# Kernel optimization log

Hardware: AMD Instinct MI355X
Metric: run time of the kernel (lower is better)

## Reference

```python
import jax, jax.numpy as jnp
import numpy as np

D_MODEL = 1024
NUM_HEADS = 16
D_K = D_MODEL // NUM_HEADS
SCALE = float(np.sqrt(D_K))


def setup_inputs() -> dict:
    key = jax.random.key(0)
    ks = jax.random.split(key, 11)
    B, S, D = 4, 2048, D_MODEL
    w_std = 1.0 / np.sqrt(D)
    inp = {
        "query": jax.random.normal(ks[0], (B, S, D), jnp.float32),
        "key": jax.random.normal(ks[1], (B, S, D), jnp.float32),
        "value": jax.random.normal(ks[2], (B, S, D), jnp.float32),
        "wq": jax.random.normal(ks[3], (D, D), jnp.float32) * w_std,
        "bq": jax.random.normal(ks[4], (D,), jnp.float32) * w_std,
        "wk": jax.random.normal(ks[5], (D, D), jnp.float32) * w_std,
        "bk": jax.random.normal(ks[6], (D,), jnp.float32) * w_std,
        "wv": jax.random.normal(ks[7], (D, D), jnp.float32) * w_std,
        "bv": jax.random.normal(ks[8], (D,), jnp.float32) * w_std,
        "wo": jax.random.normal(ks[9], (D, D), jnp.float32) * w_std,
        "bo": jax.random.normal(ks[10], (D,), jnp.float32) * w_std,
    }
    return inp


def reference(query, key, value, wq, bq, wk, bk, wv, bv, wo, bo):
    B, Sq, D = query.shape
    H, dk = NUM_HEADS, D_K
    # linear projections (weights stored as [in, out])
    q = query @ wq + bq
    k = key @ wk + bk
    v = value @ wv + bv
    # [B, H, S, d_k]
    q = q.reshape(B, Sq, H, dk).transpose(0, 2, 1, 3)
    k = k.reshape(B, -1, H, dk).transpose(0, 2, 1, 3)
    v = v.reshape(B, -1, H, dk).transpose(0, 2, 1, 3)
    # full attention scores [B, H, Sq, Sk]
    att = jnp.einsum("bhqd,bhkd->bhqk", q, k) / SCALE
    att = jax.nn.softmax(att, axis=-1)
    out = jnp.einsum("bhqk,bhkd->bhqd", att, v)
    out = out.transpose(0, 2, 1, 3).reshape(B, Sq, D)
    return out @ wo + bo
```

## Files before the change

kernel.cpp:

```cpp
#include <hip/hip_runtime.h>


typedef _Float16 fp16;
typedef fp16  fp16x8 __attribute__((ext_vector_type(8)));
typedef fp16  fp16x4 __attribute__((ext_vector_type(4)));
typedef float f32x4  __attribute__((ext_vector_type(4)));

#define NROWS 8192
#define DM    1024
#define SEQ   2048
#define DK    64
#define LOG2E 1.44269504088896340736f
#define QSCALE (0.125f * LOG2E)

__device__ __forceinline__ f32x4 mfma16x16(fp16x8 a, fp16x8 b, f32x4 c) {
    return __builtin_amdgcn_mfma_f32_16x16x32_f16(a, b, c, 0, 0, 0);
}

__device__ __forceinline__ void gload16(const fp16* g, fp16* l) {
    __builtin_amdgcn_global_load_lds(
        (const __attribute__((address_space(1))) void*)g,
        (__attribute__((address_space(3))) void*)l, 16, 0, 0);
}

__global__ __launch_bounds__(256) void cast_fp16_kernel(
    const float* __restrict__ x0, const float* __restrict__ x1,
    const float* __restrict__ x2,
    fp16* __restrict__ y0, fp16* __restrict__ y1, fp16* __restrict__ y2,
    int n4) {
    const int z = blockIdx.y;
    const float* x = (z == 0) ? x0 : (z == 1) ? x1 : x2;
    fp16*       y = (z == 0) ? y0 : (z == 1) ? y1 : y2;
    int i = blockIdx.x * 256 + threadIdx.x;
    if (i >= n4) return;
    const float4 v = ((const float4*)x)[i];
    fp16x4 o;
    o[0] = (fp16)v.x; o[1] = (fp16)v.y; o[2] = (fp16)v.z; o[3] = (fp16)v.w;
    ((fp16x4*)y)[i] = o;
}

__global__ __launch_bounds__(256) void transpose_w_kernel(
    const float* __restrict__ w0, const float* __restrict__ w1,
    const float* __restrict__ w2, const float* __restrict__ w3,
    fp16* __restrict__ t0, fp16* __restrict__ t1,
    fp16* __restrict__ t2, fp16* __restrict__ t3) {
    const int z = blockIdx.z;
    const float* W = (z == 0) ? w0 : (z == 1) ? w1 : (z == 2) ? w2 : w3;
    fp16*       T = (z == 0) ? t0 : (z == 1) ? t1 : (z == 2) ? t2 : t3;
    __shared__ float tile[32][33];
    const int tx = threadIdx.x, ty = threadIdx.y;
    const int bx = blockIdx.x * 32, by = blockIdx.y * 32;
#pragma unroll
    for (int j = 0; j < 4; ++j)
        tile[ty + 8 * j][tx] = W[(size_t)(by + ty + 8 * j) * DM + bx + tx];
    __syncthreads();
#pragma unroll
    for (int j = 0; j < 4; ++j)
        T[(size_t)(bx + ty + 8 * j) * DM + by + tx] = (fp16)tile[tx][ty + 8 * j];
}

__global__ __launch_bounds__(256) void gemm_qkv_kernel(
    const fp16* __restrict__ Xq, const fp16* __restrict__ Xk,
    const fp16* __restrict__ Xv,
    const fp16* __restrict__ Wq, const fp16* __restrict__ Wk,
    const fp16* __restrict__ Wv,
    const float* __restrict__ bq, const float* __restrict__ bk,
    const float* __restrict__ bv,
    fp16* __restrict__ Qb, fp16* __restrict__ Kb, fp16* __restrict__ Vtg,
    int zbase) {
    const int z = blockIdx.z + zbase;
    const fp16* __restrict__ A = (z == 0) ? Xq : (z == 1) ? Xk : Xv;
    const fp16* __restrict__ B = (z == 0) ? Wq : (z == 1) ? Wk : Wv;
    const float* __restrict__ bias = (z == 0) ? bq : (z == 1) ? bk : bv;
    fp16* __restrict__ outp = (z == 0) ? Qb : (z == 1) ? Kb : Vtg;
    const float oscale = (z == 0) ? QSCALE : 1.0f;

    const int tid = threadIdx.x;
    const int lane = tid & 63;
    const int w = tid >> 6;
    const int wr = w >> 1, wc = w & 1;
    const int li = lane & 15, lg = lane >> 4;
    const int m0 = blockIdx.y * 128, n0 = blockIdx.x * 128;
    const int lrow = lane >> 3;
    const int lch  = (lane & 7) ^ lrow;

    __shared__ fp16 At[128 * 64];
    __shared__ fp16 Bt[128 * 64];

    f32x4 acc[4][4] = {};

    for (int k0 = 0; k0 < DM; k0 += 64) {
        __syncthreads();
#pragma unroll
        for (int it = 0; it < 4; ++it) {
            int R = (w * 4 + it) * 8 + lrow;
            gload16(&A[(size_t)(m0 + R) * DM + k0 + lch * 8], &At[(w * 4 + it) * 512]);
            gload16(&B[(size_t)(n0 + R) * DM + k0 + lch * 8], &Bt[(w * 4 + it) * 512]);
        }
        __syncthreads();
        fp16x8 af[4][2], bfr[4][2];
#pragma unroll
        for (int mf = 0; mf < 4; ++mf)
#pragma unroll
            for (int ks = 0; ks < 2; ++ks)
                af[mf][ks] = *(const fp16x8*)&At[(wr * 64 + mf * 16 + li) * 64 +
                                                 (((ks * 4 + lg) ^ (li & 7)) * 8)];
#pragma unroll
        for (int nf = 0; nf < 4; ++nf)
#pragma unroll
            for (int ks = 0; ks < 2; ++ks)
                bfr[nf][ks] = *(const fp16x8*)&Bt[(wc * 64 + nf * 16 + li) * 64 +
                                                  (((ks * 4 + lg) ^ (li & 7)) * 8)];
#pragma unroll
        for (int ks = 0; ks < 2; ++ks)
#pragma unroll
            for (int mf = 0; mf < 4; ++mf)
#pragma unroll
                for (int nf = 0; nf < 4; ++nf)
                    acc[mf][nf] = mfma16x16(af[mf][ks], bfr[nf][ks], acc[mf][nf]);
    }
#pragma unroll
    for (int nf = 0; nf < 4; ++nf) {
        int col = n0 + wc * 64 + nf * 16 + li;
        float bv_ = bias[col];
        if (z == 2) {
#pragma unroll
            for (int mf = 0; mf < 4; ++mf) {
                int rowb = m0 + wr * 64 + mf * 16 + lg * 4;
                fp16x4 pk;
#pragma unroll
                for (int r = 0; r < 4; ++r)
                    pk[r] = (fp16)(acc[mf][nf][r] + bv_);
                size_t o = ((size_t)(rowb >> 11) * 1024 + col) * SEQ + (rowb & 2047);
                *(fp16x4*)&outp[o] = pk;
            }
        } else {
#pragma unroll
            for (int mf = 0; mf < 4; ++mf)
#pragma unroll
                for (int r = 0; r < 4; ++r) {
                    int row = m0 + wr * 64 + mf * 16 + lg * 4 + r;
                    outp[(size_t)row * DM + col] = (fp16)((acc[mf][nf][r] + bv_) * oscale);
                }
        }
    }
}

__global__ __launch_bounds__(256) void gemm_out_kernel(
    const fp16* __restrict__ A, const fp16* __restrict__ B,
    const float* __restrict__ bias, float* __restrict__ outp) {
    const int tid = threadIdx.x;
    const int lane = tid & 63;
    const int w = tid >> 6;
    const int wr = w >> 1, wc = w & 1;
    const int li = lane & 15, lg = lane >> 4;
    const int m0 = blockIdx.y * 128, n0 = blockIdx.x * 64;
    const int lrow = lane >> 3;
    const int lch  = (lane & 7) ^ lrow;

    __shared__ fp16 At[128 * 64];
    __shared__ fp16 Bt[64 * 64];

    f32x4 acc[4][2] = {};

    for (int k0 = 0; k0 < DM; k0 += 64) {
        __syncthreads();
#pragma unroll
        for (int it = 0; it < 4; ++it) {
            int R = (w * 4 + it) * 8 + lrow;
            gload16(&A[(size_t)(m0 + R) * DM + k0 + lch * 8], &At[(w * 4 + it) * 512]);
            if (it < 2) {
                int Rb = (w * 2 + it) * 8 + lrow;
                gload16(&B[(size_t)(n0 + Rb) * DM + k0 + lch * 8], &Bt[(w * 2 + it) * 512]);
            }
        }
        __syncthreads();
        fp16x8 af[4][2], bfr[2][2];
#pragma unroll
        for (int mf = 0; mf < 4; ++mf)
#pragma unroll
            for (int ks = 0; ks < 2; ++ks)
                af[mf][ks] = *(const fp16x8*)&At[(wr * 64 + mf * 16 + li) * 64 +
                                                 (((ks * 4 + lg) ^ (li & 7)) * 8)];
#pragma unroll
        for (int nf = 0; nf < 2; ++nf)
#pragma unroll
            for (int ks = 0; ks < 2; ++ks)
                bfr[nf][ks] = *(const fp16x8*)&Bt[(wc * 32 + nf * 16 + li) * 64 +
                                                  (((ks * 4 + lg) ^ (li & 7)) * 8)];
#pragma unroll
        for (int ks = 0; ks < 2; ++ks)
#pragma unroll
            for (int mf = 0; mf < 4; ++mf)
#pragma unroll
                for (int nf = 0; nf < 2; ++nf)
                    acc[mf][nf] = mfma16x16(af[mf][ks], bfr[nf][ks], acc[mf][nf]);
    }
#pragma unroll
    for (int nf = 0; nf < 2; ++nf) {
        int col = n0 + wc * 32 + nf * 16 + li;
        float bv_ = bias[col];
#pragma unroll
        for (int mf = 0; mf < 4; ++mf)
#pragma unroll
            for (int r = 0; r < 4; ++r) {
                int row = m0 + wr * 64 + mf * 16 + lg * 4 + r;
                outp[(size_t)row * DM + col] = acc[mf][nf][r] + bv_;
            }
    }
}

__global__ __launch_bounds__(512) void attn_kernel(
    const fp16* __restrict__ Qb, const fp16* __restrict__ Kb,
    const fp16* __restrict__ Vtg, fp16* __restrict__ Of) {
    const int tid = threadIdx.x;
    const int lane = tid & 63;
    const int w = tid >> 6;
    const int li = lane & 15, lg = lane >> 4;

    int L = blockIdx.x;
    L = (L & 7) * 64 + (L >> 3);
    const int qt = L & 7, bh = L >> 3;
    const int b = bh >> 4, h = bh & 15;
    const size_t rowQ = (size_t)b * SEQ + (size_t)qt * 256;
    const int c0 = h * DK;

    __shared__ fp16 Kt[2][64 * 64];
    __shared__ fp16 Vt[2][64 * 64];
    __shared__ fp16 Pl[8][32 * 64];

    fp16x8 qf[2][2];
#pragma unroll
    for (int mf = 0; mf < 2; ++mf)
#pragma unroll
        for (int ks = 0; ks < 2; ++ks)
            qf[mf][ks] = *(const fp16x8*)&Qb[(rowQ + w * 32 + mf * 16 + li) * DM +
                                             c0 + ks * 32 + lg * 8];

    fp16x8 ones;
#pragma unroll
    for (int j = 0; j < 8; ++j) ones[j] = (fp16)1.0f;

    f32x4 oacc[2][4] = {};
    f32x4 lacc[2] = {};

    const int sr = tid >> 3, sc = tid & 7;
    const int ssl = sc ^ (sr & 7);
    fp16x8 rk, rv;
    rk = *(const fp16x8*)&Kb[((size_t)b * SEQ + sr) * DM + c0 + sc * 8];
    rv = *(const fp16x8*)&Vtg[((size_t)bh * 64 + sr) * SEQ + sc * 8];
    *(fp16x8*)&Kt[0][sr * 64 + ssl * 8] = rk;
    *(fp16x8*)&Vt[0][sr * 64 + ssl * 8] = rv;
    __syncthreads();

    for (int kt = 0; kt < SEQ / 64; ++kt) {
        const int cur = kt & 1;
        const bool more = (kt + 1 < SEQ / 64);
        if (more) {
            rk = *(const fp16x8*)&Kb[((size_t)b * SEQ + (kt + 1) * 64 + sr) * DM + c0 + sc * 8];
            rv = *(const fp16x8*)&Vtg[((size_t)bh * 64 + sr) * SEQ + (kt + 1) * 64 + sc * 8];
        }

        f32x4 s[4][2] = {};
        __builtin_amdgcn_s_setprio(1);
#pragma unroll
        for (int nf = 0; nf < 4; ++nf)
#pragma unroll
            for (int ks = 0; ks < 2; ++ks) {
                fp16x8 kf = *(const fp16x8*)&Kt[cur][(nf * 16 + li) * 64 +
                                                     (((ks * 4 + lg) ^ (li & 7)) * 8)];
#pragma unroll
                for (int mf = 0; mf < 2; ++mf)
                    s[nf][mf] = mfma16x16(kf, qf[mf][ks], s[nf][mf]);
            }
        __builtin_amdgcn_s_setprio(0);

#pragma unroll
        for (int mf = 0; mf < 2; ++mf) {
            fp16x4 pk[4];
#pragma unroll
            for (int nf = 0; nf < 4; ++nf)
#pragma unroll
                for (int r = 0; r < 4; ++r)
                    pk[nf][r] = (fp16)__builtin_amdgcn_exp2f(s[nf][mf][r]);
            int row = mf * 16 + li;
#pragma unroll
            for (int nf = 0; nf < 4; ++nf) {
                int sl = (nf * 2 + (lg >> 1)) ^ (li & 7);
                *(fp16x4*)&Pl[w][row * 64 + sl * 8 + (lg & 1) * 4] = pk[nf];
            }
        }

        __builtin_amdgcn_s_setprio(1);
#pragma unroll
        for (int ks = 0; ks < 2; ++ks) {
            fp16x8 pf[2];
#pragma unroll
            for (int mf = 0; mf < 2; ++mf) {
                pf[mf] = *(const fp16x8*)&Pl[w][(mf * 16 + li) * 64 +
                                                (((ks * 4 + lg) ^ (li & 7)) * 8)];
                lacc[mf] = mfma16x16(pf[mf], ones, lacc[mf]);
            }
#pragma unroll
            for (int nf = 0; nf < 4; ++nf) {
                fp16x8 vf = *(const fp16x8*)&Vt[cur][(nf * 16 + li) * 64 +
                                                     (((ks * 4 + lg) ^ (li & 7)) * 8)];
#pragma unroll
                for (int mf = 0; mf < 2; ++mf)
                    oacc[mf][nf] = mfma16x16(pf[mf], vf, oacc[mf][nf]);
            }
        }
        __builtin_amdgcn_s_setprio(0);

        if (more) {
            *(fp16x8*)&Kt[cur ^ 1][sr * 64 + ssl * 8] = rk;
            *(fp16x8*)&Vt[cur ^ 1][sr * 64 + ssl * 8] = rv;
            __syncthreads();
        }
    }

#pragma unroll
    for (int mf = 0; mf < 2; ++mf) {
#pragma unroll
        for (int r = 0; r < 4; ++r) {
            float linv = 1.0f / lacc[mf][r];
            size_t row = rowQ + w * 32 + mf * 16 + lg * 4 + r;
#pragma unroll
            for (int nf = 0; nf < 4; ++nf) {
                int col = c0 + nf * 16 + li;
                Of[row * DM + col] = (fp16)(oacc[mf][nf][r] * linv);
            }
        }
    }
}

extern "C" void kernel_launch(void* const* d_in, const int* in_sizes, int n_in,
                              void* d_out, int out_size, void* d_ws, size_t ws_size,
                              hipStream_t stream) {
    const float* query = (const float*)d_in[0];
    const float* key   = (const float*)d_in[1];
    const float* value = (const float*)d_in[2];
    const float* wq    = (const float*)d_in[3];
    const float* bq    = (const float*)d_in[4];
    const float* wk    = (const float*)d_in[5];
    const float* bk    = (const float*)d_in[6];
    const float* wv    = (const float*)d_in[7];
    const float* bv    = (const float*)d_in[8];
    const float* wo    = (const float*)d_in[9];
    const float* bo    = (const float*)d_in[10];

    char* ws = (char*)d_ws;
    const size_t SZX = (size_t)NROWS * DM * 2;
    const size_t SZW = (size_t)DM * DM * 2;
    const int n4 = NROWS * DM / 4;
    const dim3 bT(32, 8);

    if (ws_size >= 3 * SZX + 4 * SZW + 3 * SZX) {
        fp16* Xq  = (fp16*)(ws);
        fp16* Xk  = (fp16*)(ws + SZX);
        fp16* Xv  = (fp16*)(ws + 2 * SZX);
        fp16* Wtq = (fp16*)(ws + 3 * SZX);
        fp16* Wtk = (fp16*)(ws + 3 * SZX + SZW);
        fp16* Wtv = (fp16*)(ws + 3 * SZX + 2 * SZW);
        fp16* Wto = (fp16*)(ws + 3 * SZX + 3 * SZW);
        fp16* Qb  = (fp16*)(ws + 3 * SZX + 4 * SZW);
        fp16* Kb  = (fp16*)(ws + 4 * SZX + 4 * SZW);
        fp16* Vtg = (fp16*)(ws + 5 * SZX + 4 * SZW);
        fp16* Of  = Xq;

        cast_fp16_kernel<<<dim3(8192, 3), 256, 0, stream>>>(
            query, key, value, Xq, Xk, Xv, n4);
        transpose_w_kernel<<<dim3(32, 32, 4), bT, 0, stream>>>(
            wq, wk, wv, wo, Wtq, Wtk, Wtv, Wto);
        gemm_qkv_kernel<<<dim3(8, 64, 3), 256, 0, stream>>>(
            Xq, Xk, Xv, Wtq, Wtk, Wtv, bq, bk, bv, Qb, Kb, Vtg, 0);
        attn_kernel<<<512, 512, 0, stream>>>(Qb, Kb, Vtg, Of);
        gemm_out_kernel<<<dim3(16, 64), 256, 0, stream>>>(Of, Wto, bo, (float*)d_out);
    } else {
        fp16* Xb  = (fp16*)(ws);
        fp16* Wt  = (fp16*)(ws + SZX);
        fp16* Qb  = (fp16*)(ws + SZX + SZW);
        fp16* Kb  = (fp16*)(ws + 2 * SZX + SZW);
        fp16* Vtg = (fp16*)(ws + 3 * SZX + SZW);
        fp16* Of  = Xb;

        cast_fp16_kernel<<<dim3(8192, 1), 256, 0, stream>>>(
            query, nullptr, nullptr, Xb, nullptr, nullptr, n4);
        transpose_w_kernel<<<dim3(32, 32, 1), bT, 0, stream>>>(
            wq, wq, wq, wq, Wt, Wt, Wt, Wt);
        gemm_qkv_kernel<<<dim3(8, 64, 1), 256, 0, stream>>>(
            Xb, Xb, Xb, Wt, Wt, Wt, bq, bq, bq, Qb, Qb, Qb, 0);
        cast_fp16_kernel<<<dim3(8192, 1), 256, 0, stream>>>(
            key, nullptr, nullptr, Xb, nullptr, nullptr, n4);
        transpose_w_kernel<<<dim3(32, 32, 1), bT, 0, stream>>>(
            wk, wk, wk, wk, Wt, Wt, Wt, Wt);
        gemm_qkv_kernel<<<dim3(8, 64, 1), 256, 0, stream>>>(
            Xb, Xb, Xb, Wt, Wt, Wt, bk, bk, bk, Kb, Kb, Kb, 1);
        cast_fp16_kernel<<<dim3(8192, 1), 256, 0, stream>>>(
            value, nullptr, nullptr, Xb, nullptr, nullptr, n4);
        transpose_w_kernel<<<dim3(32, 32, 1), bT, 0, stream>>>(
            wv, wv, wv, wv, Wt, Wt, Wt, Wt);
        gemm_qkv_kernel<<<dim3(8, 64, 1), 256, 0, stream>>>(
            Xb, Xb, Xb, Wt, Wt, Wt, bv, bv, bv, Vtg, Vtg, Vtg, 2);
        attn_kernel<<<512, 512, 0, stream>>>(Qb, Kb, Vtg, Of);
        transpose_w_kernel<<<dim3(32, 32, 1), bT, 0, stream>>>(
            wo, wo, wo, wo, Wt, Wt, Wt, Wt);
        gemm_out_kernel<<<dim3(16, 64), 256, 0, stream>>>(Of, Wt, bo, (float*)d_out);
    }
}
```

Baseline: 227.8 us.

## Fuse fp32-to-fp16 input cast into QKV GEMM and remap blocks per XCD

```diff
diff --git a/kernel.cpp b/kernel.cpp
--- a/kernel.cpp
+++ b/kernel.cpp
@@ -4,6 +4,7 @@
 typedef _Float16 fp16;
 typedef fp16  fp16x8 __attribute__((ext_vector_type(8)));
 typedef fp16  fp16x4 __attribute__((ext_vector_type(4)));
+typedef __fp16 h16x2 __attribute__((ext_vector_type(2)));
 typedef float f32x4  __attribute__((ext_vector_type(4)));
 
 #define NROWS 8192
@@ -17,26 +18,21 @@
     return __builtin_amdgcn_mfma_f32_16x16x32_f16(a, b, c, 0, 0, 0);
 }
 
-__device__ __forceinline__ void gload16(const fp16* g, fp16* l) {
+__device__ __forceinline__ void gload16(const void* g, void* l) {
     __builtin_amdgcn_global_load_lds(
         (const __attribute__((address_space(1))) void*)g,
         (__attribute__((address_space(3))) void*)l, 16, 0, 0);
 }
 
-__global__ __launch_bounds__(256) void cast_fp16_kernel(
-    const float* __restrict__ x0, const float* __restrict__ x1,
-    const float* __restrict__ x2,
-    fp16* __restrict__ y0, fp16* __restrict__ y1, fp16* __restrict__ y2,
-    int n4) {
-    const int z = blockIdx.y;
-    const float* x = (z == 0) ? x0 : (z == 1) ? x1 : x2;
-    fp16*       y = (z == 0) ? y0 : (z == 1) ? y1 : y2;
-    int i = blockIdx.x * 256 + threadIdx.x;
-    if (i >= n4) return;
-    const float4 v = ((const float4*)x)[i];
-    fp16x4 o;
-    o[0] = (fp16)v.x; o[1] = (fp16)v.y; o[2] = (fp16)v.z; o[3] = (fp16)v.w;
-    ((fp16x4*)y)[i] = o;
+__device__ __forceinline__ fp16x8 cvt8(f32x4 a, f32x4 b) {
+    h16x2 r0 = __builtin_amdgcn_cvt_pkrtz(a[0], a[1]);
+    h16x2 r1 = __builtin_amdgcn_cvt_pkrtz(a[2], a[3]);
+    h16x2 r2 = __builtin_amdgcn_cvt_pkrtz(b[0], b[1]);
+    h16x2 r3 = __builtin_amdgcn_cvt_pkrtz(b[2], b[3]);
+    fp16x8 v;
+    v[0] = (fp16)r0[0]; v[1] = (fp16)r0[1]; v[2] = (fp16)r1[0]; v[3] = (fp16)r1[1];
+    v[4] = (fp16)r2[0]; v[5] = (fp16)r2[1]; v[6] = (fp16)r3[0]; v[7] = (fp16)r3[1];
+    return v;
 }
 
 __global__ __launch_bounds__(256) void transpose_w_kernel(
@@ -60,16 +56,20 @@
 }
 
 __global__ __launch_bounds__(256) void gemm_qkv_kernel(
-    const fp16* __restrict__ Xq, const fp16* __restrict__ Xk,
-    const fp16* __restrict__ Xv,
+    const float* __restrict__ Xq, const float* __restrict__ Xk,
+    const float* __restrict__ Xv,
     const fp16* __restrict__ Wq, const fp16* __restrict__ Wk,
     const fp16* __restrict__ Wv,
     const float* __restrict__ bq, const float* __restrict__ bk,
     const float* __restrict__ bv,
-    fp16* __restrict__ Qb, fp16* __restrict__ Kb, fp16* __restrict__ Vtg,
-    int zbase) {
-    const int z = blockIdx.z + zbase;
-    const fp16* __restrict__ A = (z == 0) ? Xq : (z == 1) ? Xk : Xv;
+    fp16* __restrict__ Qb, fp16* __restrict__ Kb, fp16* __restrict__ Vtg) {
+    const int i = blockIdx.x;
+    const int xcd = i & 7, r = i >> 3;
+    const int z = r >> 6, rr = r & 63;
+    const int m0 = (xcd * 8 + (rr >> 3)) * 128;
+    const int n0 = (rr & 7) * 128;
+
+    const float* __restrict__ A = (z == 0) ? Xq : (z == 1) ? Xk : Xv;
     const fp16* __restrict__ B = (z == 0) ? Wq : (z == 1) ? Wk : Wv;
     const float* __restrict__ bias = (z == 0) ? bq : (z == 1) ? bk : bv;
     fp16* __restrict__ outp = (z == 0) ? Qb : (z == 1) ? Kb : Vtg;
@@ -80,31 +80,41 @@
     const int w = tid >> 6;
     const int wr = w >> 1, wc = w & 1;
     const int li = lane & 15, lg = lane >> 4;
-    const int m0 = blockIdx.y * 128, n0 = blockIdx.x * 128;
-    const int lrow = lane >> 3;
-    const int lch  = (lane & 7) ^ lrow;
-
-    __shared__ fp16 At[128 * 64];
-    __shared__ fp16 Bt[128 * 64];
+    const int lrow8 = lane >> 3;
+    const int lch8  = (lane & 7) ^ lrow8;
+    const int lrow4 = lane >> 4;
+    const int lch16 = (lane & 15);
+
+    __shared__ float Atf[128 * 64];
+    __shared__ fp16  Bt[128 * 64];
 
     f32x4 acc[4][4] = {};
 
     for (int k0 = 0; k0 < DM; k0 += 64) {
         __syncthreads();
 #pragma unroll
+        for (int it = 0; it < 8; ++it) {
+            int R = (w * 8 + it) * 4 + lrow4;
+            gload16(&A[(size_t)(m0 + R) * DM + k0 + ((lch16 ^ (R & 15)) * 4)],
+                    &Atf[(w * 8 + it) * 256]);
+        }
+#pragma unroll
         for (int it = 0; it < 4; ++it) {
-            int R = (w * 4 + it) * 8 + lrow;
-            gload16(&A[(size_t)(m0 + R) * DM + k0 + lch * 8], &At[(w * 4 + it) * 512]);
-            gload16(&B[(size_t)(n0 + R) * DM + k0 + lch * 8], &Bt[(w * 4 + it) * 512]);
+            int R = (w * 4 + it) * 8 + lrow8;
+            gload16(&B[(size_t)(n0 + R) * DM + k0 + lch8 * 8], &Bt[(w * 4 + it) * 512]);
         }
         __syncthreads();
         fp16x8 af[4][2], bfr[4][2];
 #pragma unroll
         for (int mf = 0; mf < 4; ++mf)
 #pragma unroll
-            for (int ks = 0; ks < 2; ++ks)
-                af[mf][ks] = *(const fp16x8*)&At[(wr * 64 + mf * 16 + li) * 64 +
-                                                 (((ks * 4 + lg) ^ (li & 7)) * 8)];
+            for (int ks = 0; ks < 2; ++ks) {
+                int R = wr * 64 + mf * 16 + li;
+                int g0 = ks * 8 + lg * 2;
+                f32x4 a0 = *(const f32x4*)&Atf[R * 64 + ((g0 ^ li) * 4)];
+                f32x4 a1 = *(const f32x4*)&Atf[R * 64 + (((g0 + 1) ^ li) * 4)];
+                af[mf][ks] = cvt8(a0, a1);
+            }
 #pragma unroll
         for (int nf = 0; nf < 4; ++nf)
 #pragma unroll
@@ -129,8 +139,8 @@
                 int rowb = m0 + wr * 64 + mf * 16 + lg * 4;
                 fp16x4 pk;
 #pragma unroll
-                for (int r = 0; r < 4; ++r)
-                    pk[r] = (fp16)(acc[mf][nf][r] + bv_);
+                for (int r2 = 0; r2 < 4; ++r2)
+                    pk[r2] = (fp16)(acc[mf][nf][r2] + bv_);
                 size_t o = ((size_t)(rowb >> 11) * 1024 + col) * SEQ + (rowb & 2047);
                 *(fp16x4*)&outp[o] = pk;
             }
@@ -138,9 +148,9 @@
 #pragma unroll
             for (int mf = 0; mf < 4; ++mf)
 #pragma unroll
-                for (int r = 0; r < 4; ++r) {
-                    int row = m0 + wr * 64 + mf * 16 + lg * 4 + r;
-                    outp[(size_t)row * DM + col] = (fp16)((acc[mf][nf][r] + bv_) * oscale);
+                for (int r2 = 0; r2 < 4; ++r2) {
+                    int row = m0 + wr * 64 + mf * 16 + lg * 4 + r2;
+                    outp[(size_t)row * DM + col] = (fp16)((acc[mf][nf][r2] + bv_) * oscale);
                 }
         }
     }
@@ -149,12 +159,16 @@
 __global__ __launch_bounds__(256) void gemm_out_kernel(
     const fp16* __restrict__ A, const fp16* __restrict__ B,
     const float* __restrict__ bias, float* __restrict__ outp) {
+    const int i = blockIdx.x;
+    const int xcd = i & 7, r = i >> 3;
+    const int m0 = (xcd * 8 + (r >> 4)) * 128;
+    const int n0 = (r & 15) * 64;
+
     const int tid = threadIdx.x;
     const int lane = tid & 63;
     const int w = tid >> 6;
     const int wr = w >> 1, wc = w & 1;
     const int li = lane & 15, lg = lane >> 4;
-    const int m0 = blockIdx.y * 128, n0 = blockIdx.x * 64;
     const int lrow = lane >> 3;
     const int lch  = (lane & 7) ^ lrow;
 
@@ -203,9 +217,9 @@
 #pragma unroll
         for (int mf = 0; mf < 4; ++mf)
 #pragma unroll
-            for (int r = 0; r < 4; ++r) {
-                int row = m0 + wr * 64 + mf * 16 + lg * 4 + r;
-                outp[(size_t)row * DM + col] = acc[mf][nf][r] + bv_;
+            for (int r2 = 0; r2 < 4; ++r2) {
+                int row = m0 + wr * 64 + mf * 16 + lg * 4 + r2;
+                outp[(size_t)row * DM + col] = acc[mf][nf][r2] + bv_;
             }
     }
 }
@@ -352,59 +366,21 @@
     char* ws = (char*)d_ws;
     const size_t SZX = (size_t)NROWS * DM * 2;
     const size_t SZW = (size_t)DM * DM * 2;
-    const int n4 = NROWS * DM / 4;
+    fp16* Wtq = (fp16*)(ws);
+    fp16* Wtk = (fp16*)(ws + SZW);
+    fp16* Wtv = (fp16*)(ws + 2 * SZW);
+    fp16* Wto = (fp16*)(ws + 3 * SZW);
+    fp16* Qb  = (fp16*)(ws + 4 * SZW);
+    fp16* Kb  = (fp16*)(ws + 4 * SZW + SZX);
+    fp16* Vtg = (fp16*)(ws + 4 * SZW + 2 * SZX);
+    fp16* Of  = (fp16*)(ws + 4 * SZW + 3 * SZX);
+
     const dim3 bT(32, 8);
 
-    if (ws_size >= 3 * SZX + 4 * SZW + 3 * SZX) {
-        fp16* Xq  = (fp16*)(ws);
-        fp16* Xk  = (fp16*)(ws + SZX);
-        fp16* Xv  = (fp16*)(ws + 2 * SZX);
-        fp16* Wtq = (fp16*)(ws + 3 * SZX);
-        fp16* Wtk = (fp16*)(ws + 3 * SZX + SZW);
-        fp16* Wtv = (fp16*)(ws + 3 * SZX + 2 * SZW);
-        fp16* Wto = (fp16*)(ws + 3 * SZX + 3 * SZW);
-        fp16* Qb  = (fp16*)(ws + 3 * SZX + 4 * SZW);
-        fp16* Kb  = (fp16*)(ws + 4 * SZX + 4 * SZW);
-        fp16* Vtg = (fp16*)(ws + 5 * SZX + 4 * SZW);
-        fp16* Of  = Xq;
-
-        cast_fp16_kernel<<<dim3(8192, 3), 256, 0, stream>>>(
-            query, key, value, Xq, Xk, Xv, n4);
-        transpose_w_kernel<<<dim3(32, 32, 4), bT, 0, stream>>>(
-            wq, wk, wv, wo, Wtq, Wtk, Wtv, Wto);
-        gemm_qkv_kernel<<<dim3(8, 64, 3), 256, 0, stream>>>(
-            Xq, Xk, Xv, Wtq, Wtk, Wtv, bq, bk, bv, Qb, Kb, Vtg, 0);
-        attn_kernel<<<512, 512, 0, stream>>>(Qb, Kb, Vtg, Of);
-        gemm_out_kernel<<<dim3(16, 64), 256, 0, stream>>>(Of, Wto, bo, (float*)d_out);
-    } else {
-        fp16* Xb  = (fp16*)(ws);
-        fp16* Wt  = (fp16*)(ws + SZX);
-        fp16* Qb  = (fp16*)(ws + SZX + SZW);
-        fp16* Kb  = (fp16*)(ws + 2 * SZX + SZW);
-        fp16* Vtg = (fp16*)(ws + 3 * SZX + SZW);
-        fp16* Of  = Xb;
-
-        cast_fp16_kernel<<<dim3(8192, 1), 256, 0, stream>>>(
-            query, nullptr, nullptr, Xb, nullptr, nullptr, n4);
-        transpose_w_kernel<<<dim3(32, 32, 1), bT, 0, stream>>>(
-            wq, wq, wq, wq, Wt, Wt, Wt, Wt);
-        gemm_qkv_kernel<<<dim3(8, 64, 1), 256, 0, stream>>>(
-            Xb, Xb, Xb, Wt, Wt, Wt, bq, bq, bq, Qb, Qb, Qb, 0);
-        cast_fp16_kernel<<<dim3(8192, 1), 256, 0, stream>>>(
-            key, nullptr, nullptr, Xb, nullptr, nullptr, n4);
-        transpose_w_kernel<<<dim3(32, 32, 1), bT, 0, stream>>>(
-            wk, wk, wk, wk, Wt, Wt, Wt, Wt);
-        gemm_qkv_kernel<<<dim3(8, 64, 1), 256, 0, stream>>>(
-            Xb, Xb, Xb, Wt, Wt, Wt, bk, bk, bk, Kb, Kb, Kb, 1);
-        cast_fp16_kernel<<<dim3(8192, 1), 256, 0, stream>>>(
-            value, nullptr, nullptr, Xb, nullptr, nullptr, n4);
-        transpose_w_kernel<<<dim3(32, 32, 1), bT, 0, stream>>>(
-            wv, wv, wv, wv, Wt, Wt, Wt, Wt);
-        gemm_qkv_kernel<<<dim3(8, 64, 1), 256, 0, stream>>>(
-            Xb, Xb, Xb, Wt, Wt, Wt, bv, bv, bv, Vtg, Vtg, Vtg, 2);
-        attn_kernel<<<512, 512, 0, stream>>>(Qb, Kb, Vtg, Of);
-        transpose_w_kernel<<<dim3(32, 32, 1), bT, 0, stream>>>(
-            wo, wo, wo, wo, Wt, Wt, Wt, Wt);
-        gemm_out_kernel<<<dim3(16, 64), 256, 0, stream>>>(Of, Wt, bo, (float*)d_out);
-    }
-}
+    transpose_w_kernel<<<dim3(32, 32, 4), bT, 0, stream>>>(
+        wq, wk, wv, wo, Wtq, Wtk, Wtv, Wto);
+    gemm_qkv_kernel<<<1536, 256, 0, stream>>>(
+        query, key, value, Wtq, Wtk, Wtv, bq, bk, bv, Qb, Kb, Vtg);
+    attn_kernel<<<512, 512, 0, stream>>>(Qb, Kb, Vtg, Of);
+    gemm_out_kernel<<<1024, 256, 0, stream>>>(Of, Wto, bo, (float*)d_out);
+}
```

Result: faster. 192.2 us (-15.6%).
